# Performance work log

Hardware: AMD Instinct MI355X
Metric: run time of the kernel (lower is better)

Reference implementation:

```python
import jax, jax.numpy as jnp
import numpy as np

B, S, D, H = 4, 1024, 1024, 16
HD = D // H  # 64
NEG = -10000000.0


def setup_inputs() -> dict:
    key = jax.random.key(0)
    ks = jax.random.split(key, 8)
    x = jax.random.normal(ks[0], (B, S, D), dtype=jnp.float32)
    adj = jax.random.randint(ks[1], (B, S, S), 0, 2).astype(jnp.float32)
    scale = 1.0 / np.sqrt(D)
    Wq = jax.random.normal(ks[2], (D, D), dtype=jnp.float32) * scale
    bq = jnp.zeros((D,), dtype=jnp.float32)
    Wk = jax.random.normal(ks[3], (D, D), dtype=jnp.float32) * scale
    bk = jnp.zeros((D,), dtype=jnp.float32)
    Wv = jax.random.normal(ks[4], (D, D), dtype=jnp.float32) * scale
    bv = jnp.zeros((D,), dtype=jnp.float32)
    return {"x": x, "adj": adj, "Wq": Wq, "bq": bq, "Wk": Wk, "bk": bk, "Wv": Wv, "bv": bv}


def reference(x, adj, Wq, bq, Wk, bk, Wv, bv):
    # QKV projections, split into heads: [B,S,D] -> [B,H,S,HD]
    def heads(t):
        return t.reshape(B, S, H, HD).transpose(0, 2, 1, 3)

    q = heads(x @ Wq + bq)
    k = heads(x @ Wk + bk)
    v = heads(x @ Wv + bv)

    # scaled scores [B,H,S,S]
    scores = jnp.einsum('bhqd,bhkd->bhqk', q, k) / jnp.sqrt(jnp.asarray(HD, x.dtype))
    # adjacency mask: 0 where adj>=0.5 else -1e7, broadcast over heads
    mask_add = jnp.where(adj < 0.5, jnp.asarray(NEG, x.dtype), jnp.asarray(0.0, x.dtype))
    scores = scores + mask_add[:, None, :, :]

    probs = jax.nn.softmax(scores, axis=-1)
    ctx = jnp.einsum('bhqk,bhkd->bhqd', probs, v)  # [B,H,S,HD]
    ctx = ctx.transpose(0, 2, 1, 3).reshape(B, S, D)
    h = jax.nn.relu(ctx)
    return (h, adj)
```

## Files before the change

kernel.cpp:

```cpp
#include <hip/hip_runtime.h>

constexpr int Bn  = 4;
constexpr int Sn  = 1024;
constexpr int Dn  = 1024;
constexpr int Hn  = 16;
constexpr int HDn = 64;

using short8   = __attribute__((ext_vector_type(8))) short;
using float4v  = __attribute__((ext_vector_type(4))) float;
using float16v = __attribute__((ext_vector_type(16))) float;

__device__ __forceinline__ ushort f2bf(float f) {
    union { float f; unsigned u; } v; v.f = f;
    unsigned r = v.u + 0x7fff + ((v.u >> 16) & 1);
    return (ushort)(r >> 16);
}

__device__ __forceinline__ void gload16(const void* g, void* l) {
    __builtin_amdgcn_global_load_lds(
        (const __attribute__((address_space(1))) void*)g,
        (__attribute__((address_space(3))) void*)l, 16, 0, 0);
}

__global__ __launch_bounds__(256) void prep(
    const float* __restrict__ x,
    const float* __restrict__ Wq, const float* __restrict__ Wk,
    const float* __restrict__ Wv, const float* __restrict__ adj,
    ushort* __restrict__ xb, ushort* __restrict__ Wt, uint* __restrict__ Mb,
    float* __restrict__ out)
{
    const int bx  = blockIdx.x;
    const int tid = threadIdx.x;
    __shared__ __align__(16) ushort pool[64 * 72];

    if (bx < 2048) {
        const size_t i = ((size_t)bx * 256 + tid) * 8;
        float4 a = *(const float4*)&x[i];
        float4 b = *(const float4*)&x[i + 4];
        ushort o[8] = {f2bf(a.x), f2bf(a.y), f2bf(a.z), f2bf(a.w),
                       f2bf(b.x), f2bf(b.y), f2bf(b.z), f2bf(b.w)};
        *(uint4*)&xb[i] = *(const uint4*)o;
    } else if (bx < 2816) {
        const int idx = bx - 2048;
        const int which = idx >> 8, rem = idx & 255;
        const float* __restrict__ W = (which == 0) ? Wq : (which == 1) ? Wk : Wv;
        ushort* __restrict__ O = Wt + (size_t)which * Dn * Dn;
        const int k0 = (rem & 15) * 64, n0 = (rem >> 4) * 64;
        ushort* T = pool;

        const int kl = tid >> 4, nl = (tid & 15) * 4;
#pragma unroll
        for (int p = 0; p < 4; ++p) {
            float4 w4 = *(const float4*)&W[(size_t)(k0 + p * 16 + kl) * Dn + n0 + nl];
            T[(nl + 0) * 72 + p * 16 + kl] = f2bf(w4.x);
            T[(nl + 1) * 72 + p * 16 + kl] = f2bf(w4.y);
            T[(nl + 2) * 72 + p * 16 + kl] = f2bf(w4.z);
            T[(nl + 3) * 72 + p * 16 + kl] = f2bf(w4.w);
        }
        __syncthreads();
        const int nr = tid >> 2, kc = (tid & 3) * 16;
        uint4 u0 = *(const uint4*)&T[nr * 72 + kc];
        uint4 u1 = *(const uint4*)&T[nr * 72 + kc + 8];
        *(uint4*)&O[(size_t)(n0 + nr) * Dn + k0 + kc]     = u0;
        *(uint4*)&O[(size_t)(n0 + nr) * Dn + k0 + kc + 8] = u1;
    } else {
        const int idx = bx - 2816;
        const int kt = idx & 15, qt = (idx >> 4) & 7, b = idx >> 7;
        char* msk = (char*)pool;

        float* ocopy = out + (size_t)Bn * Sn * Dn;
        const int r16 = tid >> 4, c4 = (tid & 15) * 4;
#pragma unroll
        for (int p = 0; p < 8; ++p) {
            const int row = p * 16 + r16;
            const size_t gi = ((size_t)b * Sn + qt * 128 + row) * Sn + kt * 64 + c4;
            float4 a = *(const float4*)&adj[gi];
            *(float4*)&ocopy[gi] = a;
            char* mr = &msk[row * 68 + c4];
            mr[0] = a.x >= 0.5f; mr[1] = a.y >= 0.5f;
            mr[2] = a.z >= 0.5f; mr[3] = a.w >= 0.5f;
        }
        __syncthreads();

        const int lane = tid & 63, w = tid >> 6;
        const int col = lane & 31, hi = lane >> 5;
        uint words[16];
#pragma unroll
        for (int mt = 0; mt < 2; ++mt)
#pragma unroll
            for (int pr = 0; pr < 8; ++pr) {
                const int r0 = 2 * pr;
                const int kl = mt * 32 + (r0 & 3) + 8 * (r0 >> 2) + 4 * hi;
                const char* mr = &msk[(w * 32 + col) * 68];
                words[mt * 8 + pr] = (mr[kl]     ? 0x0000FFFFu : 0u) |
                                     (mr[kl + 1] ? 0xFFFF0000u : 0u);
            }
        uint* dst = Mb + ((((size_t)(b * 8 + qt) * 16 + kt) * 4 + w) * 64 + lane) * 16;
#pragma unroll
        for (int c = 0; c < 4; ++c)
            *(uint4*)&dst[c * 4] =
                make_uint4(words[c*4], words[c*4+1], words[c*4+2], words[c*4+3]);
    }
}

__global__ __launch_bounds__(256) void qkv_gemm(
    const ushort* __restrict__ xb, const ushort* __restrict__ Wt,
    const float* __restrict__ bq, const float* __restrict__ bk,
    const float* __restrict__ bv,
    ushort* __restrict__ Qb, ushort* __restrict__ Kb, ushort* __restrict__ Vb)
{
    const int n  = blockIdx.x;
    const int v  = (n & 7) * 96 + (n >> 3);
    const int by = v / 24;
    const int rr = v - by * 24;
    const int bxi   = rr & 7;
    const int which = rr >> 3;

    const ushort* __restrict__ Bw   = Wt + (size_t)which * Dn * Dn;
    const float* __restrict__  bias = (which == 0) ? bq : (which == 1) ? bk : bv;
    ushort* __restrict__       Out  = (which == 0) ? Qb : (which == 1) ? Kb : Vb;
    const float scale = (which == 0) ? 0.18033688011112042f : 1.0f;

    const int n0   = bxi * 128;
    const int m0   = by * 128;
    const int tid  = threadIdx.x;
    const int wave = tid >> 6;
    const int lane = tid & 63;
    const int wm   = wave >> 1;
    const int wn   = wave & 1;

    __shared__ __align__(16) ushort As[128 * 32];
    __shared__ __align__(16) ushort Bs[128 * 32];

    const int L0 = wave * 64 + lane;
    const int r0s = L0 >> 2, c0s = ((L0 & 3) ^ ((L0 >> 3) & 3)) * 8;
    const int L1 = L0 + 256;
    const int r1s = L1 >> 2, c1s = ((L1 & 3) ^ ((L1 >> 3) & 3)) * 8;

    const ushort* pA0 = &xb[(size_t)(m0 + r0s) * Dn + c0s];
    const ushort* pA1 = &xb[(size_t)(m0 + r1s) * Dn + c1s];
    const ushort* pB0 = &Bw[(size_t)(n0 + r0s) * Dn + c0s];
    const ushort* pB1 = &Bw[(size_t)(n0 + r1s) * Dn + c1s];

    char* ldsA0 = (char*)As + wave * 1024;
    char* ldsA1 = (char*)As + wave * 1024 + 4096;
    char* ldsB0 = (char*)Bs + wave * 1024;
    char* ldsB1 = (char*)Bs + wave * 1024 + 4096;

    const int mlane = lane & 15;
    const int kg = (((lane >> 4) ^ ((mlane >> 1) & 3))) * 8;

    float4v acc[4][4];
    const float4v z4 = {0.f, 0.f, 0.f, 0.f};
#pragma unroll
    for (int i = 0; i < 4; ++i)
#pragma unroll
        for (int j = 0; j < 4; ++j) acc[i][j] = z4;

    for (int k0 = 0; k0 < Dn; k0 += 32) {
        __syncthreads();
        gload16(pA0, ldsA0);
        gload16(pA1, ldsA1);
        gload16(pB0, ldsB0);
        gload16(pB1, ldsB1);
        pA0 += 32; pA1 += 32; pB0 += 32; pB1 += 32;
        __syncthreads();

        short8 af[4], bf[4];
#pragma unroll
        for (int i = 0; i < 4; ++i)
            af[i] = *(const short8*)&As[(wm * 64 + i * 16 + mlane) * 32 + kg];
#pragma unroll
        for (int j = 0; j < 4; ++j)
            bf[j] = *(const short8*)&Bs[(wn * 64 + j * 16 + mlane) * 32 + kg];
#pragma unroll
        for (int i = 0; i < 4; ++i)
#pragma unroll
            for (int j = 0; j < 4; ++j)
                acc[i][j] = __builtin_amdgcn_mfma_f32_16x16x32_bf16(af[i], bf[j], acc[i][j], 0, 0, 0);
    }

    const int rb  = (lane >> 4) * 4;
    const int col = lane & 15;
#pragma unroll
    for (int j = 0; j < 4; ++j) {
        const int nn = n0 + wn * 64 + j * 16 + col;
        const float bias_n = bias[nn];
        const int h  = nn >> 6;
        const int hd = nn & 63;
#pragma unroll
        for (int i = 0; i < 4; ++i) {
#pragma unroll
            for (int r = 0; r < 4; ++r) {
                const int m = m0 + wm * 64 + i * 16 + rb + r;
                const int b = m >> 10;
                const int s = m & 1023;
                size_t addr;
                if (which == 2)
                    addr = (((size_t)(b * Hn + h)) * HDn + hd) * Sn + s;
                else
                    addr = (((size_t)(b * Hn + h)) * Sn + s) * HDn + hd;
                Out[addr] = f2bf((acc[i][j][r] + bias_n) * scale);
            }
        }
    }
}

__global__ __launch_bounds__(512, 4) void attn_mfma(
    const ushort* __restrict__ Q, const ushort* __restrict__ K,
    const ushort* __restrict__ Vt, const uint* __restrict__ Mw,
    float* __restrict__ out)
{
    const int n  = blockIdx.x;
    const int qt = (n >> 3) & 7;
    const int bh = (n & 7) | ((n >> 6) << 3);
    const int h  = bh & 15;
    const int b  = bh >> 4;

    const int tid  = threadIdx.x;
    const int w    = tid >> 6, lane = tid & 63;
    const int g    = w >> 2;
    const int wq   = w & 3;
    const int col  = lane & 31, hi = lane >> 5;

    const size_t hb = ((size_t)(b * Hn + h)) * Sn * HDn;
    const ushort* Kg = K + hb;
    const ushort* Vg = Vt + hb;

    __shared__ __align__(16) ushort KV[2][2][2][64 * 72];

    short8 qf[4];
#pragma unroll
    for (int kp = 0; kp < 4; ++kp)
        qf[kp] = *(const short8*)&Q[hb +
            (size_t)(qt * 128 + wq * 32 + col) * HDn + kp * 16 + hi * 8];

    float16v o_[2];
#pragma unroll
    for (int dt = 0; dt < 2; ++dt)
#pragma unroll
        for (int r = 0; r < 16; ++r) o_[dt][r] = 0.f;
    float ls = 0.f;

    const int t  = tid & 255;
    const int c0 = t, c1 = t + 256;
    const int la0 = (c0 >> 3) * 72 + (c0 & 7) * 8;
    const int la1 = (c1 >> 3) * 72 + (c1 & 7) * 8;
    const int kb  = g * 8;

    uint4 k0 = *(const uint4*)&Kg[(size_t)(kb * 64 + (c0 >> 3)) * HDn + (c0 & 7) * 8];
    uint4 k1 = *(const uint4*)&Kg[(size_t)(kb * 64 + (c1 >> 3)) * HDn + (c1 & 7) * 8];
    uint4 v0 = *(const uint4*)&Vg[(size_t)(c0 >> 3) * Sn + kb * 64 + (c0 & 7) * 8];
    uint4 v1 = *(const uint4*)&Vg[(size_t)(c1 >> 3) * Sn + kb * 64 + (c1 & 7) * 8];
    *(uint4*)&KV[g][0][0][la0] = k0;  *(uint4*)&KV[g][0][0][la1] = k1;
    *(uint4*)&KV[g][0][1][la0] = v0;  *(uint4*)&KV[g][0][1][la1] = v1;
    __syncthreads();

    const uint* mbase = Mw + ((size_t)((b * 8 + qt) * 16) * 4 + wq) * 1024 + lane * 16;

    for (int kt = 0; kt < 8; ++kt) {
        const int cur = kt & 1;
        if (kt < 7) {
            const int nk = (kb + kt + 1) * 64;
            k0 = *(const uint4*)&Kg[(size_t)(nk + (c0 >> 3)) * HDn + (c0 & 7) * 8];
            k1 = *(const uint4*)&Kg[(size_t)(nk + (c1 >> 3)) * HDn + (c1 & 7) * 8];
            v0 = *(const uint4*)&Vg[(size_t)(c0 >> 3) * Sn + nk + (c0 & 7) * 8];
            v1 = *(const uint4*)&Vg[(size_t)(c1 >> 3) * Sn + nk + (c1 & 7) * 8];
        }
        const uint* mp = mbase + (size_t)(kb + kt) * 4096;
        uint4 mk4[4];
        mk4[0] = *(const uint4*)(mp);
        mk4[1] = *(const uint4*)(mp + 4);
        mk4[2] = *(const uint4*)(mp + 8);
        mk4[3] = *(const uint4*)(mp + 12);
        const uint* mka = (const uint*)mk4;

#pragma unroll
        for (int mt = 0; mt < 2; ++mt) {
            float16v s_;
#pragma unroll
            for (int r = 0; r < 16; ++r) s_[r] = 0.f;
            __builtin_amdgcn_s_setprio(1);
#pragma unroll
            for (int kp = 0; kp < 4; ++kp) {
                short8 ak = *(const short8*)&KV[g][cur][0][(mt * 32 + col) * 72 + kp * 16 + hi * 8];
                s_ = __builtin_amdgcn_mfma_f32_32x32x16_bf16(ak, qf[kp], s_, 0, 0, 0);
            }
            __builtin_amdgcn_s_setprio(0);

            unsigned up[8];
#pragma unroll
            for (int pr = 0; pr < 8; ++pr) {
                const unsigned e0 = __float_as_uint(exp2f(s_[2 * pr]))     + 0x8000u;
                const unsigned e1 = __float_as_uint(exp2f(s_[2 * pr + 1])) + 0x8000u;
                const unsigned u  = __builtin_amdgcn_perm(e1, e0, 0x07060302u) & mka[mt * 8 + pr];
                up[pr] = u;
                ls += __uint_as_float(u << 16) + __uint_as_float(u & 0xffff0000u);
            }

            __builtin_amdgcn_s_setprio(1);
#pragma unroll
            for (int kh = 0; kh < 2; ++kh) {
                auto s02 = __builtin_amdgcn_permlane32_swap(
                    up[kh * 4 + 0], up[kh * 4 + 2], false, false);
                auto s13 = __builtin_amdgcn_permlane32_swap(
                    up[kh * 4 + 1], up[kh * 4 + 3], false, false);
                union { short8 s; unsigned u[4]; } f;
                f.u[0] = s02[0];
                f.u[1] = s13[0];
                f.u[2] = s02[1];
                f.u[3] = s13[1];
                const int kp = mt * 2 + kh;
#pragma unroll
                for (int dt = 0; dt < 2; ++dt) {
                    short8 av = *(const short8*)&KV[g][cur][1][(dt * 32 + col) * 72 + kp * 16 + hi * 8];
                    o_[dt] = __builtin_amdgcn_mfma_f32_32x32x16_bf16(av, f.s, o_[dt], 0, 0, 0);
                }
            }
            __builtin_amdgcn_s_setprio(0);
        }

        if (kt < 7) {
            const int nxt = cur ^ 1;
            *(uint4*)&KV[g][nxt][0][la0] = k0;  *(uint4*)&KV[g][nxt][0][la1] = k1;
            *(uint4*)&KV[g][nxt][1][la0] = v0;  *(uint4*)&KV[g][nxt][1][la1] = v1;
        }
        __syncthreads();
    }

    float* xo  = (float*)&KV[0][0][0][0];
    float* lsx = xo + 4 * 64 * 36;
    if (g == 1) {
        float* dst = &xo[(wq * 64 + lane) * 36];
#pragma unroll
        for (int dt = 0; dt < 2; ++dt)
#pragma unroll
            for (int r4 = 0; r4 < 4; ++r4) {
                float4 o4 = make_float4(o_[dt][r4 * 4 + 0], o_[dt][r4 * 4 + 1],
                                        o_[dt][r4 * 4 + 2], o_[dt][r4 * 4 + 3]);
                *(float4*)&dst[dt * 16 + r4 * 4] = o4;
            }
        lsx[wq * 64 + lane] = ls;
    }
    __syncthreads();
    if (g == 0) {
        const float* src = &xo[(wq * 64 + lane) * 36];
        const float lt = ls + lsx[wq * 64 + lane];
        const float l  = lt + (float)__shfl_xor(lt, 32, 64);
        const float inv = 1.0f / l;
        const int q = qt * 128 + wq * 32 + col;
        float* op = &out[((size_t)b * Sn + q) * Dn + h * 64];
#pragma unroll
        for (int dt = 0; dt < 2; ++dt)
#pragma unroll
            for (int rg = 0; rg < 4; ++rg) {
                float4 s4 = *(const float4*)&src[dt * 16 + rg * 4];
                const int d = dt * 32 + rg * 8 + hi * 4;
                float4 o4;
                o4.x = fmaxf((o_[dt][rg * 4 + 0] + s4.x) * inv, 0.0f);
                o4.y = fmaxf((o_[dt][rg * 4 + 1] + s4.y) * inv, 0.0f);
                o4.z = fmaxf((o_[dt][rg * 4 + 2] + s4.z) * inv, 0.0f);
                o4.w = fmaxf((o_[dt][rg * 4 + 3] + s4.w) * inv, 0.0f);
                *(float4*)&op[d] = o4;
            }
    }
}

extern "C" void kernel_launch(void* const* d_in, const int* in_sizes, int n_in,
                              void* d_out, int out_size, void* d_ws, size_t ws_size,
                              hipStream_t stream)
{
    const float* x   = (const float*)d_in[0];
    const float* adj = (const float*)d_in[1];
    const float* Wq  = (const float*)d_in[2];
    const float* bq  = (const float*)d_in[3];
    const float* Wk  = (const float*)d_in[4];
    const float* bk  = (const float*)d_in[5];
    const float* Wv  = (const float*)d_in[6];
    const float* bv  = (const float*)d_in[7];
    float* out = (float*)d_out;

    ushort* xb = (ushort*)d_ws;
    ushort* Wt = xb + (size_t)Bn * Sn * Dn;
    ushort* Qb = Wt + (size_t)3 * Dn * Dn;
    ushort* Kb = Qb + (size_t)Bn * Hn * Sn * HDn;
    ushort* Vb = Kb + (size_t)Bn * Hn * Sn * HDn;
    uint*   Mb = (uint*)(Vb + (size_t)Bn * Hn * Sn * HDn);

    prep<<<dim3(3328), 256, 0, stream>>>(x, Wq, Wk, Wv, adj, xb, Wt, Mb, out);

    qkv_gemm<<<dim3(768), 256, 0, stream>>>(xb, Wt, bq, bk, bv, Qb, Kb, Vb);

    attn_mfma<<<dim3(512), 512, 0, stream>>>(Qb, Kb, Vb, Mb, out);
}
```

Measured before the change: 182.5 us.

## Double-buffer LDS tiles in QKV projection GEMM to overlap loads with MFMA

The QKV projection GEMM now keeps two LDS buffers for the A and B tiles. It issues the global-to-LDS loads for the next K-step before running the MFMAs on the current one, and needs one barrier per iteration instead of two. This is meant to hide global load latency behind matrix-core work. The cost is double the LDS for that kernel, which could lower occupancy. The speedup also depends on the barrier waiting for the async loads.

```diff
diff --git a/kernel.cpp b/kernel.cpp
--- a/kernel.cpp
+++ b/kernel.cpp
@@ -129,8 +129,8 @@
     const int wm   = wave >> 1;
     const int wn   = wave & 1;
 
-    __shared__ __align__(16) ushort As[128 * 32];
-    __shared__ __align__(16) ushort Bs[128 * 32];
+    __shared__ __align__(16) ushort As[2][128 * 32];
+    __shared__ __align__(16) ushort Bs[2][128 * 32];
 
     const int L0 = wave * 64 + lane;
     const int r0s = L0 >> 2, c0s = ((L0 & 3) ^ ((L0 >> 3) & 3)) * 8;
@@ -142,10 +142,13 @@
     const ushort* pB0 = &Bw[(size_t)(n0 + r0s) * Dn + c0s];
     const ushort* pB1 = &Bw[(size_t)(n0 + r1s) * Dn + c1s];
 
-    char* ldsA0 = (char*)As + wave * 1024;
-    char* ldsA1 = (char*)As + wave * 1024 + 4096;
-    char* ldsB0 = (char*)Bs + wave * 1024;
-    char* ldsB1 = (char*)Bs + wave * 1024 + 4096;
+    char* ldsA = (char*)As + wave * 1024 + (lane & 63) * 16;
+    char* ldsB = (char*)Bs + wave * 1024 + (lane & 63) * 16;
+    char* ldsA0b = (char*)As + wave * 1024;
+    char* ldsA1b = (char*)As + wave * 1024 + 4096;
+    char* ldsB0b = (char*)Bs + wave * 1024;
+    char* ldsB1b = (char*)Bs + wave * 1024 + 4096;
+    (void)ldsA; (void)ldsB;
 
     const int mlane = lane & 15;
     const int kg = (((lane >> 4) ^ ((mlane >> 1) & 3))) * 8;
@@ -157,27 +160,38 @@
 #pragma unroll
         for (int j = 0; j < 4; ++j) acc[i][j] = z4;
 
+    gload16(pA0, ldsA0b);
+    gload16(pA1, ldsA1b);
+    gload16(pB0, ldsB0b);
+    gload16(pB1, ldsB1b);
+    pA0 += 32; pA1 += 32; pB0 += 32; pB1 += 32;
+    __syncthreads();
+
     for (int k0 = 0; k0 < Dn; k0 += 32) {
-        __syncthreads();
-        gload16(pA0, ldsA0);
-        gload16(pA1, ldsA1);
-        gload16(pB0, ldsB0);
-        gload16(pB1, ldsB1);
-        pA0 += 32; pA1 += 32; pB0 += 32; pB1 += 32;
-        __syncthreads();
+        const int cur = (k0 >> 5) & 1;
+        const int nxt = cur ^ 1;
+        if (k0 + 32 < Dn) {
+            gload16(pA0, ldsA0b + nxt * 8192);
+            gload16(pA1, ldsA1b + nxt * 8192);
+            gload16(pB0, ldsB0b + nxt * 8192);
+            gload16(pB1, ldsB1b + nxt * 8192);
+            pA0 += 32; pA1 += 32; pB0 += 32; pB1 += 32;
+        }
 
         short8 af[4], bf[4];
 #pragma unroll
         for (int i = 0; i < 4; ++i)
-            af[i] = *(const short8*)&As[(wm * 64 + i * 16 + mlane) * 32 + kg];
+            af[i] = *(const short8*)&As[cur][(wm * 64 + i * 16 + mlane) * 32 + kg];
 #pragma unroll
         for (int j = 0; j < 4; ++j)
-            bf[j] = *(const short8*)&Bs[(wn * 64 + j * 16 + mlane) * 32 + kg];
+            bf[j] = *(const short8*)&Bs[cur][(wn * 64 + j * 16 + mlane) * 32 + kg];
 #pragma unroll
         for (int i = 0; i < 4; ++i)
 #pragma unroll
             for (int j = 0; j < 4; ++j)
                 acc[i][j] = __builtin_amdgcn_mfma_f32_16x16x32_bf16(af[i], bf[j], acc[i][j], 0, 0, 0);
+
+        __syncthreads();
     }
 
     const int rb  = (lane >> 4) * 4;
```

Result: no change. 181.5 us (-0.6%).

## Triple-buffer LDS tiles in QKV projection GEMM with async prefetch pipeline

Applied to the files above, without the earlier changes.

The QKV GEMM k-loop now uses three LDS buffers and issues global-to-LDS loads two tiles ahead, waiting with explicit vmcnt counts. Before, every iteration loaded a tile and stalled on it before computing. This should hide global memory latency behind the MFMA work. It also raises MFMA issue priority with s_setprio. The cost is triple the LDS footprint, which may lower occupancy, plus hand-managed wait counts that are fragile.

```diff
diff --git a/kernel.cpp b/kernel.cpp
--- a/kernel.cpp
+++ b/kernel.cpp
@@ -129,8 +129,8 @@
     const int wm   = wave >> 1;
     const int wn   = wave & 1;
 
-    __shared__ __align__(16) ushort As[128 * 32];
-    __shared__ __align__(16) ushort Bs[128 * 32];
+    __shared__ __align__(16) ushort As[3][128 * 32];
+    __shared__ __align__(16) ushort Bs[3][128 * 32];
 
     const int L0 = wave * 64 + lane;
     const int r0s = L0 >> 2, c0s = ((L0 & 3) ^ ((L0 >> 3) & 3)) * 8;
@@ -142,11 +142,6 @@
     const ushort* pB0 = &Bw[(size_t)(n0 + r0s) * Dn + c0s];
     const ushort* pB1 = &Bw[(size_t)(n0 + r1s) * Dn + c1s];
 
-    char* ldsA0 = (char*)As + wave * 1024;
-    char* ldsA1 = (char*)As + wave * 1024 + 4096;
-    char* ldsB0 = (char*)Bs + wave * 1024;
-    char* ldsB1 = (char*)Bs + wave * 1024 + 4096;
-
     const int mlane = lane & 15;
     const int kg = (((lane >> 4) ^ ((mlane >> 1) & 3))) * 8;
 
@@ -157,27 +152,72 @@
 #pragma unroll
         for (int j = 0; j < 4; ++j) acc[i][j] = z4;
 
-    for (int k0 = 0; k0 < Dn; k0 += 32) {
-        __syncthreads();
-        gload16(pA0, ldsA0);
-        gload16(pA1, ldsA1);
-        gload16(pB0, ldsB0);
-        gload16(pB1, ldsB1);
+    auto stage = [&](int c) {
+        char* ab = (char*)As + c * 8192 + wave * 1024;
+        char* bb = (char*)Bs + c * 8192 + wave * 1024;
+        gload16(pA0, ab);
+        gload16(pA1, ab + 4096);
+        gload16(pB0, bb);
+        gload16(pB1, bb + 4096);
         pA0 += 32; pA1 += 32; pB0 += 32; pB1 += 32;
-        __syncthreads();
-
-        short8 af[4], bf[4];
+    };
+    auto ldsread = [&](int c, short8 (&af)[4], short8 (&bf)[4]) {
 #pragma unroll
         for (int i = 0; i < 4; ++i)
-            af[i] = *(const short8*)&As[(wm * 64 + i * 16 + mlane) * 32 + kg];
+            af[i] = *(const short8*)&As[c][(wm * 64 + i * 16 + mlane) * 32 + kg];
 #pragma unroll
         for (int j = 0; j < 4; ++j)
-            bf[j] = *(const short8*)&Bs[(wn * 64 + j * 16 + mlane) * 32 + kg];
+            bf[j] = *(const short8*)&Bs[c][(wn * 64 + j * 16 + mlane) * 32 + kg];
+    };
+    auto domfma = [&](short8 (&af)[4], short8 (&bf)[4]) {
+        __builtin_amdgcn_s_setprio(1);
 #pragma unroll
         for (int i = 0; i < 4; ++i)
 #pragma unroll
             for (int j = 0; j < 4; ++j)
                 acc[i][j] = __builtin_amdgcn_mfma_f32_16x16x32_bf16(af[i], bf[j], acc[i][j], 0, 0, 0);
+        __builtin_amdgcn_s_setprio(0);
+    };
+
+    stage(0); stage(1); stage(2);
+
+    constexpr int NT = Dn / 32;
+    int cur = 0;
+    for (int k = 0; k < NT - 3; ++k) {
+        asm volatile("s_waitcnt vmcnt(8)" ::: "memory");
+        __builtin_amdgcn_s_barrier();
+        short8 af[4], bf[4];
+        ldsread(cur, af, bf);
+        asm volatile("s_waitcnt lgkmcnt(0)" ::: "memory");
+        __builtin_amdgcn_sched_barrier(0);
+        __builtin_amdgcn_s_barrier();
+        __builtin_amdgcn_sched_barrier(0);
+        stage(cur);
+        domfma(af, bf);
+        cur = (cur == 2) ? 0 : cur + 1;
+    }
+    {
+        asm volatile("s_waitcnt vmcnt(8)" ::: "memory");
+        __builtin_amdgcn_s_barrier();
+        short8 af[4], bf[4];
+        ldsread(cur, af, bf);
+        domfma(af, bf);
+        cur = (cur == 2) ? 0 : cur + 1;
+    }
+    {
+        asm volatile("s_waitcnt vmcnt(4)" ::: "memory");
+        __builtin_amdgcn_s_barrier();
+        short8 af[4], bf[4];
+        ldsread(cur, af, bf);
+        domfma(af, bf);
+        cur = (cur == 2) ? 0 : cur + 1;
+    }
+    {
+        asm volatile("s_waitcnt vmcnt(0)" ::: "memory");
+        __builtin_amdgcn_s_barrier();
+        short8 af[4], bf[4];
+        ldsread(cur, af, bf);
+        domfma(af, bf);
     }
 
     const int rb  = (lane >> 4) * 4;
```

New measurement: 183.7 us. No clear change (+0.7%).

## Double-buffer A tile in LDS and load B fragments directly to registers

Applied to the files above, without the earlier changes.

Restructures the QKV projection GEMM main loop to double-buffer the activation tile in LDS, using manual vmcnt waits and split barriers so global loads for step k+2 overlap the MFMAs of step k. The weight tile no longer goes through LDS; each wave loads its B fragments straight from global memory into registers one step ahead, ping-ponging between two register sets. MFMA sections also run at raised wave priority. This aims to hide global latency and halve per-step LDS traffic. The cost is more registers and uncoalesced-ish direct global reads of weights, and it relies on the hand-written vmcnt count being correct.

```diff
diff --git a/kernel.cpp b/kernel.cpp
--- a/kernel.cpp
+++ b/kernel.cpp
@@ -129,26 +129,21 @@
     const int wm   = wave >> 1;
     const int wn   = wave & 1;
 
-    __shared__ __align__(16) ushort As[128 * 32];
-    __shared__ __align__(16) ushort Bs[128 * 32];
-
-    const int L0 = wave * 64 + lane;
+    __shared__ __align__(16) ushort As[2][128 * 32];
+
+    const int L0 = tid;
     const int r0s = L0 >> 2, c0s = ((L0 & 3) ^ ((L0 >> 3) & 3)) * 8;
-    const int L1 = L0 + 256;
+    const int L1 = tid + 256;
     const int r1s = L1 >> 2, c1s = ((L1 & 3) ^ ((L1 >> 3) & 3)) * 8;
 
     const ushort* pA0 = &xb[(size_t)(m0 + r0s) * Dn + c0s];
     const ushort* pA1 = &xb[(size_t)(m0 + r1s) * Dn + c1s];
-    const ushort* pB0 = &Bw[(size_t)(n0 + r0s) * Dn + c0s];
-    const ushort* pB1 = &Bw[(size_t)(n0 + r1s) * Dn + c1s];
-
-    char* ldsA0 = (char*)As + wave * 1024;
-    char* ldsA1 = (char*)As + wave * 1024 + 4096;
-    char* ldsB0 = (char*)Bs + wave * 1024;
-    char* ldsB1 = (char*)Bs + wave * 1024 + 4096;
 
     const int mlane = lane & 15;
-    const int kg = (((lane >> 4) ^ ((mlane >> 1) & 3))) * 8;
+    const int kg  = (((lane >> 4) ^ ((mlane >> 1) & 3))) * 8;
+    const int kg0 = (lane >> 4) * 8;
+
+    const ushort* pB = &Bw[(size_t)(n0 + wn * 64 + mlane) * Dn + kg0];
 
     float4v acc[4][4];
     const float4v z4 = {0.f, 0.f, 0.f, 0.f};
@@ -157,27 +152,52 @@
 #pragma unroll
         for (int j = 0; j < 4; ++j) acc[i][j] = z4;
 
-    for (int k0 = 0; k0 < Dn; k0 += 32) {
-        __syncthreads();
-        gload16(pA0, ldsA0);
-        gload16(pA1, ldsA1);
-        gload16(pB0, ldsB0);
-        gload16(pB1, ldsB1);
-        pA0 += 32; pA1 += 32; pB0 += 32; pB1 += 32;
-        __syncthreads();
-
-        short8 af[4], bf[4];
+    auto stageA = [&](int c) {
+        char* ab = (char*)As + c * 8192 + wave * 1024;
+        gload16(pA0, ab);
+        gload16(pA1, ab + 4096);
+        pA0 += 32; pA1 += 32;
+    };
+
+    constexpr int NT = Dn / 32;
+
+    auto kstep = [&](int k, int cur, short8 (&bcur)[4], short8 (&bnext)[4]) {
+        asm volatile("s_waitcnt vmcnt(6)" ::: "memory");
+        __builtin_amdgcn_s_barrier();
+        __builtin_amdgcn_sched_barrier(0);
+        short8 af[4];
 #pragma unroll
         for (int i = 0; i < 4; ++i)
-            af[i] = *(const short8*)&As[(wm * 64 + i * 16 + mlane) * 32 + kg];
-#pragma unroll
-        for (int j = 0; j < 4; ++j)
-            bf[j] = *(const short8*)&Bs[(wn * 64 + j * 16 + mlane) * 32 + kg];
+            af[i] = *(const short8*)&As[cur][(wm * 64 + i * 16 + mlane) * 32 + kg];
+        asm volatile("s_waitcnt lgkmcnt(0)" ::: "memory");
+        __builtin_amdgcn_sched_barrier(0);
+        __builtin_amdgcn_s_barrier();
+        __builtin_amdgcn_sched_barrier(0);
+        if (k + 2 < NT) stageA(cur);
+        if (k + 1 < NT) {
+            const int kn = (k + 1) * 32;
+#pragma unroll
+            for (int j = 0; j < 4; ++j)
+                bnext[j] = *(const short8*)&pB[(size_t)j * 16 * Dn + kn];
+        }
+        __builtin_amdgcn_s_setprio(1);
 #pragma unroll
         for (int i = 0; i < 4; ++i)
 #pragma unroll
             for (int j = 0; j < 4; ++j)
-                acc[i][j] = __builtin_amdgcn_mfma_f32_16x16x32_bf16(af[i], bf[j], acc[i][j], 0, 0, 0);
+                acc[i][j] = __builtin_amdgcn_mfma_f32_16x16x32_bf16(af[i], bcur[j], acc[i][j], 0, 0, 0);
+        __builtin_amdgcn_s_setprio(0);
+    };
+
+    stageA(0); stageA(1);
+    short8 b0[4], b1[4];
+#pragma unroll
+    for (int j = 0; j < 4; ++j)
+        b0[j] = *(const short8*)&pB[(size_t)j * 16 * Dn];
+
+    for (int k = 0; k < NT; k += 2) {
+        kstep(k,     0, b0, b1);
+        kstep(k + 1, 1, b1, b0);
     }
 
     const int rb  = (lane >> 4) * 4;
```

New measurement: 227.4 us. +24.6%, slower.
